# Kernel tuning notes

Measured on AMD Instinct MI355X. Metric: run time of the kernel, lower is better.

Reference implementation:

```python
import jax, jax.numpy as jnp
from jax import lax
import numpy as np

# ---- dims / neuron params (match init_kwargs) ----
B, T, ENC, HID = 256, 500, 700, 128
TAU_MEM = 20.0      # tauSr == tauRef == tau_mem
THETA = 1.0         # spike_threshold
SCALE_REF = 1.0
WIDTH_GRAD = 1.0    # tauRho (surrogate width)
SCALE_GRAD = 1.0    # scaleRho (surrogate scale)


def alpha_filter(x, tau, mult):
    """Causal convolution along axis 0 with SLAYER's alpha (SRM) kernel
    h[k] = mult * (k/tau) * exp(1 - k/tau), Ts = 1.  Implemented as an exact
    2-state linear recurrence instead of an O(T^2) FIR conv.
    x: (T, ...) -> y: (T, ...)
    """
    d = jnp.exp(-1.0 / tau)          # per-step decay
    c = mult * jnp.exp(1.0) / tau    # h[k] = c * k * d**k

    def step(carry, xt):
        p, q = carry
        qn = d * q + c * d * p       # output at t (h[0] = 0)
        pn = d * p + xt
        return (pn, qn), qn

    z = jnp.zeros_like(x[0])
    _, y = lax.scan(step, (z, z), x)
    return y


def _spike_core(u):
    """SLAYER getSpikes: at each t, membrane = psp + accumulated refractory
    response (alpha kernel with mult = -2*theta*scaleRef, tau = tauRef) of all
    past spikes; emit spike (1/Ts) when membrane >= theta.
    u: (T, B, C) psp values -> (spikes, post-refractory membrane), both (T, B, C).
    """
    d = jnp.exp(-1.0 / TAU_MEM)
    c = (-2.0 * THETA * SCALE_REF) * jnp.exp(1.0) / TAU_MEM

    def step(carry, ut):
        p, q = carry
        qn = d * q + c * d * p       # refractory contribution at t (0 from spike at t)
        u_t = ut + qn                # membrane after refractory subtraction
        s_t = (u_t >= THETA).astype(ut.dtype)
        pn = d * p + s_t
        return (pn, qn), (s_t, u_t)

    z = jnp.zeros_like(u[0])
    _, (s, u_post) = lax.scan(step, (z, z), u)
    return s, u_post


@jax.custom_vjp
def spike(u):
    return _spike_core(u)[0]


def _spike_fwd(u):
    s, u_post = _spike_core(u)
    return s, u_post


def _spike_bwd(u_post, g):
    # SLAYER surrogate: pdf = scaleRho / (tauRho*theta) * exp(-|u - theta| / (tauRho*theta)),
    # evaluated on the refractory-modified membrane; grad does not flow through
    # the refractory recurrence (matches the torch autograd.Function).
    tc = WIDTH_GRAD * THETA
    pdf = (SCALE_GRAD / tc) * jnp.exp(-jnp.abs(u_post - THETA) / tc)
    return (g * pdf,)


spike.defvjp(_spike_fwd, _spike_bwd)


def setup_inputs():
    key = jax.random.key(0)
    k1, k2, k3 = jax.random.split(key, 3)
    # sparse binary input spike trains (B, T, ENC)
    x = (jax.random.uniform(k1, (B, T, ENC)) < 0.05).astype(jnp.float32)
    w1 = jax.random.normal(k2, (HID, ENC), dtype=jnp.float32) * 0.1
    w2 = jax.random.normal(k3, (1, HID), dtype=jnp.float32) * 0.3
    return {"x": x, "w1": w1, "w2": w2}


def reference(x, w1, w2):
    # x: (B, T, ENC) -> time-major (T, B, ENC) for the temporal scans
    xt = jnp.transpose(x, (1, 0, 2))
    h = jnp.einsum('tbc,hc->tbh', xt, w1)        # slayer.dense (bias-free linear per step)
    h = alpha_filter(h, TAU_MEM, 1.0)            # slayer.psp
    s1 = spike(h)                                # slayer.spike (threshold + refractory)
    o = jnp.einsum('tbh,oh->tbo', s1, w2)
    o = alpha_filter(o, TAU_MEM, 1.0)
    s2 = spike(o)
    return jnp.transpose(s2, (1, 0, 2))          # (B, T, 1), matches out2.movedim(-1, 1)
```

## Files before the change

### kernel.cpp

```cpp
#include <hip/hip_runtime.h>

#define BB  256
#define TT  500
#define ENC 700
#define ENC_PAD 704
#define HID 128

__global__ __launch_bounds__(128) void transpose_w1_kernel(const float* __restrict__ w1,
                                                           float* __restrict__ w1t) {
    int c = blockIdx.x;
    int h = threadIdx.x;
    w1t[c * HID + h] = (c < ENC) ? w1[h * ENC + c] : 0.0f;
}

__global__ __launch_bounds__(256) void spmm3_kernel(const float* __restrict__ x,
                                                    const float* __restrict__ w1t,
                                                    float* __restrict__ h) {
    __shared__ ushort lists[4][144];
    const int lane = threadIdx.x & 63;
    const int w = threadIdx.x >> 6;
    const int r = blockIdx.x * 4 + w;
    const float* xrow = x + (size_t)r * ENC;
    const unsigned long long lanemask_lt = (1ull << lane) - 1ull;

    float xv[11];
    #pragma unroll
    for (int k = 0; k < 11; ++k) {
        int c = k * 64 + lane;
        xv[k] = (c < ENC) ? xrow[c] : 0.0f;
    }

    int base = 0;
    #pragma unroll
    for (int k = 0; k < 11; ++k) {
        bool act = (xv[k] != 0.0f);
        unsigned long long m = __ballot(act);
        if (act) {
            int pos = base + (int)__popcll(m & lanemask_lt);
            if (pos < 128) lists[w][pos] = (ushort)(k * 64 + lane);
        }
        base += (int)__popcll(m);
    }
    int n = (base < 128) ? base : 128;
    int npad = (n + 15) & ~15;
    if (lane < npad - n) lists[w][n + lane] = (ushort)ENC;
    __syncthreads();

    float accx = 0.f, accy = 0.f;
    for (int j = 0; j < npad; j += 16) {
        int c0  = lists[w][j +  0], c1  = lists[w][j +  1];
        int c2  = lists[w][j +  2], c3  = lists[w][j +  3];
        int c4  = lists[w][j +  4], c5  = lists[w][j +  5];
        int c6  = lists[w][j +  6], c7  = lists[w][j +  7];
        int c8  = lists[w][j +  8], c9  = lists[w][j +  9];
        int c10 = lists[w][j + 10], c11 = lists[w][j + 11];
        int c12 = lists[w][j + 12], c13 = lists[w][j + 13];
        int c14 = lists[w][j + 14], c15 = lists[w][j + 15];
        float2 t0  = ((const float2*)(w1t + (size_t)c0  * HID))[lane];
        float2 t1  = ((const float2*)(w1t + (size_t)c1  * HID))[lane];
        float2 t2  = ((const float2*)(w1t + (size_t)c2  * HID))[lane];
        float2 t3  = ((const float2*)(w1t + (size_t)c3  * HID))[lane];
        float2 t4  = ((const float2*)(w1t + (size_t)c4  * HID))[lane];
        float2 t5  = ((const float2*)(w1t + (size_t)c5  * HID))[lane];
        float2 t6  = ((const float2*)(w1t + (size_t)c6  * HID))[lane];
        float2 t7  = ((const float2*)(w1t + (size_t)c7  * HID))[lane];
        float2 t8  = ((const float2*)(w1t + (size_t)c8  * HID))[lane];
        float2 t9  = ((const float2*)(w1t + (size_t)c9  * HID))[lane];
        float2 t10 = ((const float2*)(w1t + (size_t)c10 * HID))[lane];
        float2 t11 = ((const float2*)(w1t + (size_t)c11 * HID))[lane];
        float2 t12 = ((const float2*)(w1t + (size_t)c12 * HID))[lane];
        float2 t13 = ((const float2*)(w1t + (size_t)c13 * HID))[lane];
        float2 t14 = ((const float2*)(w1t + (size_t)c14 * HID))[lane];
        float2 t15 = ((const float2*)(w1t + (size_t)c15 * HID))[lane];
        accx += t0.x;  accy += t0.y;
        accx += t1.x;  accy += t1.y;
        accx += t2.x;  accy += t2.y;
        accx += t3.x;  accy += t3.y;
        accx += t4.x;  accy += t4.y;
        accx += t5.x;  accy += t5.y;
        accx += t6.x;  accy += t6.y;
        accx += t7.x;  accy += t7.y;
        accx += t8.x;  accy += t8.y;
        accx += t9.x;  accy += t9.y;
        accx += t10.x; accy += t10.y;
        accx += t11.x; accy += t11.y;
        accx += t12.x; accy += t12.y;
        accx += t13.x; accy += t13.y;
        accx += t14.x; accy += t14.y;
        accx += t15.x; accy += t15.y;
    }

    int b = r / TT;
    int t = r - b * TT;
    float2* dst = (float2*)(h + (size_t)t * (BB * HID) + (size_t)b * HID);
    dst[lane] = make_float2(accx, accy);
}

__device__ __forceinline__ void async_copy4(const float* g, float* l) {
    __builtin_amdgcn_global_load_lds(
        (const __attribute__((address_space(1))) void*)g,
        (__attribute__((address_space(3))) void*)l,
        4, 0, 0);
}

__global__ __launch_bounds__(128) void recur_kernel(const float* __restrict__ hgl,
                                                    const float* __restrict__ w2,
                                                    float* __restrict__ out) {
    __shared__ float hbuf[2][50 * 128];
    __shared__ float vbuf[50 * 129];
    __shared__ float pbuf[2][50];

    const int b = blockIdx.x;
    const int tid = threadIdx.x;
    const int lane = tid & 63;
    const int w = tid >> 6;

    const float D   = 0.95122942450071400910f;
    const float CD  = (float)(0.13591409142295226 * 0.95122942450071400910);
    const float CRD = (float)(-0.27182818284590452 * 0.95122942450071400910);

    float ap = 0.f, aq = 0.f, rp = 0.f, rq = 0.f;
    float Ap = 0.f, Aq = 0.f, Rp = 0.f, Rq = 0.f;
    const float w2v = w2[tid];

    auto stage = [&](int chunk, int buf) {
        const int t0 = chunk * 50 + w * 25;
        #pragma unroll 5
        for (int i = 0; i < 25; ++i) {
            const float* g = hgl + (size_t)(t0 + i) * (BB * HID) + (size_t)b * HID + lane;
            float* l = &hbuf[buf][(w * 25 + i) * 128];
            async_copy4(g, l);
            async_copy4(g + 64, l + 64);
        }
    };

    stage(0, 0);
    __syncthreads();

    for (int chunk = 0; chunk < 10; ++chunk) {
        const int cur = chunk & 1;
        if (chunk < 9) stage(chunk + 1, cur ^ 1);

        const float* hb = &hbuf[cur][0];
        #pragma unroll
        for (int tl = 0; tl < 50; ++tl) {
            float hv = hb[tl * 128 + tid];
            float y = fmaf(D, aq, CD * ap);
            aq = y;
            ap = fmaf(D, ap, hv);
            float q = fmaf(D, rq, CRD * rp);
            float u = y + q;
            float s = (u >= 1.0f) ? 1.0f : 0.0f;
            rq = q;
            rp = fmaf(D, rp, s);
            vbuf[tl * 129 + tid] = s * w2v;
        }
        __syncthreads();

        if (tid < 50) {
            const float* row = &vbuf[tid * 129];
            float a0 = 0.f, a1 = 0.f, a2 = 0.f, a3 = 0.f;
            #pragma unroll
            for (int k = 0; k < 64; k += 4) {
                a0 += row[k]; a1 += row[k + 1]; a2 += row[k + 2]; a3 += row[k + 3];
            }
            pbuf[0][tid] = (a0 + a1) + (a2 + a3);
        } else if (tid >= 64 && tid < 114) {
            const float* row = &vbuf[(tid - 64) * 129 + 64];
            float a0 = 0.f, a1 = 0.f, a2 = 0.f, a3 = 0.f;
            #pragma unroll
            for (int k = 0; k < 64; k += 4) {
                a0 += row[k]; a1 += row[k + 1]; a2 += row[k + 2]; a3 += row[k + 3];
            }
            pbuf[1][tid - 64] = (a0 + a1) + (a2 + a3);
        }
        __syncthreads();

        float my_s2 = 0.f;
        #pragma unroll
        for (int tl = 0; tl < 50; ++tl) {
            float ot = pbuf[0][tl] + pbuf[1][tl];
            float y2 = fmaf(D, Aq, CD * Ap);
            Aq = y2;
            Ap = fmaf(D, Ap, ot);
            float q2 = fmaf(D, Rq, CRD * Rp);
            float u2 = y2 + q2;
            float s2 = (u2 >= 1.0f) ? 1.0f : 0.0f;
            Rq = q2;
            Rp = fmaf(D, Rp, s2);
            if (tl == tid) my_s2 = s2;
        }
        if (tid < 50) out[(size_t)b * TT + chunk * 50 + tid] = my_s2;
    }
}

extern "C" void kernel_launch(void* const* d_in, const int* in_sizes, int n_in,
                              void* d_out, int out_size, void* d_ws, size_t ws_size,
                              hipStream_t stream) {
    const float* x  = (const float*)d_in[0];
    const float* w1 = (const float*)d_in[1];
    const float* w2 = (const float*)d_in[2];
    float* out = (float*)d_out;

    float* h   = (float*)d_ws;
    float* w1t = h + (size_t)TT * BB * HID;

    hipLaunchKernelGGL(transpose_w1_kernel, dim3(ENC_PAD), dim3(HID), 0, stream, w1, w1t);
    hipLaunchKernelGGL(spmm3_kernel, dim3((BB * TT) / 4), dim3(256), 0, stream, x, w1t, h);
    hipLaunchKernelGGL(recur_kernel, dim3(BB), dim3(128), 0, stream, h, w2, out);
}
```

Before: 616.7 us.

## Store h batch-major and prefetch recurrence inputs into registers instead of LDS

The SpMM kernel now writes h in (B,T,HID) row order, so each recurrence block reads a contiguous slab for its batch element. The recurrence kernel drops the async global-to-LDS double buffer and instead double-buffers 50 timesteps of h in two register arrays, issuing the loads for the next chunk before computing the current one. This removes LDS staging traffic and strided loads, but it costs about 100 extra VGPRs per thread and relies on the compiler keeping the loads in flight across the compute.

```diff
diff --git a/kernel.cpp b/kernel.cpp
--- a/kernel.cpp
+++ b/kernel.cpp
@@ -90,30 +90,18 @@
         accx += t15.x; accy += t15.y;
     }
 
-    int b = r / TT;
-    int t = r - b * TT;
-    float2* dst = (float2*)(h + (size_t)t * (BB * HID) + (size_t)b * HID);
+    float2* dst = (float2*)(h + (size_t)r * HID);
     dst[lane] = make_float2(accx, accy);
-}
-
-__device__ __forceinline__ void async_copy4(const float* g, float* l) {
-    __builtin_amdgcn_global_load_lds(
-        (const __attribute__((address_space(1))) void*)g,
-        (__attribute__((address_space(3))) void*)l,
-        4, 0, 0);
 }
 
 __global__ __launch_bounds__(128) void recur_kernel(const float* __restrict__ hgl,
                                                     const float* __restrict__ w2,
                                                     float* __restrict__ out) {
-    __shared__ float hbuf[2][50 * 128];
     __shared__ float vbuf[50 * 129];
     __shared__ float pbuf[2][50];
 
     const int b = blockIdx.x;
     const int tid = threadIdx.x;
-    const int lane = tid & 63;
-    const int w = tid >> 6;
 
     const float D   = 0.95122942450071400910f;
     const float CD  = (float)(0.13591409142295226 * 0.95122942450071400910);
@@ -123,31 +111,17 @@
     float Ap = 0.f, Aq = 0.f, Rp = 0.f, Rq = 0.f;
     const float w2v = w2[tid];
 
-    auto stage = [&](int chunk, int buf) {
-        const int t0 = chunk * 50 + w * 25;
-        #pragma unroll 5
-        for (int i = 0; i < 25; ++i) {
-            const float* g = hgl + (size_t)(t0 + i) * (BB * HID) + (size_t)b * HID + lane;
-            float* l = &hbuf[buf][(w * 25 + i) * 128];
-            async_copy4(g, l);
-            async_copy4(g + 64, l + 64);
-        }
-    };
-
-    stage(0, 0);
-    __syncthreads();
-
-    for (int chunk = 0; chunk < 10; ++chunk) {
-        const int cur = chunk & 1;
-        if (chunk < 9) stage(chunk + 1, cur ^ 1);
-
-        const float* hb = &hbuf[cur][0];
+    const float* hb = hgl + (size_t)b * (TT * HID) + tid;
+
+    float hA[50], hB[50];
+
+    auto body = [&](const float (&hv)[50], int chunk) {
         #pragma unroll
         for (int tl = 0; tl < 50; ++tl) {
-            float hv = hb[tl * 128 + tid];
+            float h_ = hv[tl];
             float y = fmaf(D, aq, CD * ap);
             aq = y;
-            ap = fmaf(D, ap, hv);
+            ap = fmaf(D, ap, h_);
             float q = fmaf(D, rq, CRD * rp);
             float u = y + q;
             float s = (u >= 1.0f) ? 1.0f : 0.0f;
@@ -191,6 +165,24 @@
             if (tl == tid) my_s2 = s2;
         }
         if (tid < 50) out[(size_t)b * TT + chunk * 50 + tid] = my_s2;
+    };
+
+    #pragma unroll
+    for (int j = 0; j < 50; ++j) hA[j] = hb[j * HID];
+
+    for (int cp = 0; cp < 5; ++cp) {
+        {
+            const float* g = hb + (size_t)(2 * cp + 1) * 50 * HID;
+            #pragma unroll
+            for (int j = 0; j < 50; ++j) hB[j] = g[j * HID];
+        }
+        body(hA, 2 * cp);
+        if (cp < 4) {
+            const float* g = hb + (size_t)(2 * cp + 2) * 50 * HID;
+            #pragma unroll
+            for (int j = 0; j < 50; ++j) hA[j] = g[j * HID];
+        }
+        body(hB, 2 * cp + 1);
     }
 }
 
```

Measured after the change: 603.4 us. 1.02x faster.
